# Performance work log

Hardware: AMD Instinct MI355X
Metric: run time of the kernel (lower is better)

Reference implementation:

```python
import jax, jax.numpy as jnp
import numpy as np

B, S, D, E = 32, 16, 64, 768  # batch, max summary segments, max doc splits, embed dim
EPS = 1e-12


def _l2norm(x):
    # tf.nn.l2_normalize: x * rsqrt(max(sum(x^2), eps))
    return x * jax.lax.rsqrt(jnp.maximum(jnp.sum(x * x, axis=-1, keepdims=True), EPS))


def setup_inputs() -> dict:
    key = jax.random.key(0)
    ks = jax.random.split(key, 12)
    nd = jax.random.randint(ks[0], (B,), 1, D + 1)
    ns = jax.random.randint(ks[1], (B,), 1, S + 1)
    doc = jax.random.normal(ks[2], (B, D, E), jnp.float32)
    seg = jax.random.normal(ks[3], (B, S, E), jnp.float32)
    # emulate RaggedTensor.to_tensor(): zero padding beyond ragged lengths
    doc = doc * (jnp.arange(D)[None, :, None] < nd[:, None, None])
    seg = seg * (jnp.arange(S)[None, :, None] < ns[:, None, None])
    tis = jax.random.uniform(ks[4], (B, S), jnp.float32)
    tis = jnp.where(jnp.arange(S)[None, :] < ns[:, None], tis, 1.0)
    tagg = jax.random.uniform(ks[5], (B,), jnp.float32)
    s1, s2, s3 = 1.0 / np.sqrt(2 * E), 1.0 / np.sqrt(E), 1.0 / np.sqrt(E // 2)
    W1 = jax.random.normal(ks[6], (2 * E, E), jnp.float32) * s1
    W2 = jax.random.normal(ks[7], (E, E // 2), jnp.float32) * s2
    W3 = jax.random.normal(ks[8], (E // 2, 1), jnp.float32) * s3
    return {
        'document_splits_embedding': doc,
        'summary_sentences_embedding': seg,
        'num_document_splits': nd,
        'num_summary_segments': ns,
        'target_agg_score': tagg,
        'target_instance_score': tis,
        'W1': W1, 'b1': jnp.zeros((E,), jnp.float32),
        'W2': W2, 'b2': jnp.zeros((E // 2,), jnp.float32),
        'W3': W3, 'b3': jnp.zeros((1,), jnp.float32),
    }


def reference(document_splits_embedding, summary_sentences_embedding,
              num_document_splits, num_summary_segments,
              target_agg_score, target_instance_score,
              W1, b1, W2, b2, W3, b3):
    doc, seg = document_splits_embedding, summary_sentences_embedding
    nd, ns = num_document_splits, num_summary_segments
    b, d, e = doc.shape
    s = seg.shape[1]
    nsf = ns.astype(jnp.float32)

    # target_instance_score padded with 1.0 beyond ragged length (done in setup; pass through)
    tis = target_instance_score

    # ---- pairwise MLP over all (segment, doc_split) pairs ----
    pair = jnp.concatenate([
        jnp.broadcast_to(doc[:, None, :, :], (b, s, d, e)),
        jnp.broadcast_to(seg[:, :, None, :], (b, s, d, e)),
    ], axis=-1)                                             # [B,S,D,2E]
    h = jax.nn.gelu(pair @ W1 + b1, approximate=False)      # [B,S,D,E]
    h = jax.nn.gelu(h @ W2 + b2, approximate=False)         # [B,S,D,E/2]
    mlp_out = jax.nn.sigmoid(h @ W3 + b3)[..., 0]           # [B,S,D]

    doc_mask = (jnp.arange(d)[None, :] < nd[:, None]).astype(jnp.float32)  # [B,D]
    scored = doc_mask[:, None, :] * mlp_out                # mask invalid doc splits
    pred0 = jnp.max(scored, axis=2)                         # [B,S]
    seg_scale = jnp.where(ns > 10, 1.0, 100.0)[:, None]     # faithful to mask+(1-mask)*100
    pred = seg_scale * pred0                                # [B,S]

    # ---- cosine similarity prior (keras CosineSimilarity = -cos) ----
    dn = _l2norm(doc)                                       # [B,D,E]
    sn = _l2norm(seg)                                       # [B,S,E]
    cos = jnp.einsum('bse,bde->bsd', sn, dn)                # [B,S,D]
    sim = doc_mask[:, None, :] * (1.0 + (-cos)) / 2.0
    doc_cos = jnp.max(sim, axis=2)                          # [B,S]
    seg_mask = (jnp.arange(s)[None, :] < ns[:, None]).astype(jnp.float32)
    diff = jnp.abs(doc_cos - pred) * seg_mask
    cos_prior = jnp.mean(jnp.sum(diff, axis=1) / nsf)

    # ---- correlation prior: Pearson correlation over the 768 'sample' axis ----
    c = seg - jnp.mean(seg, axis=-1, keepdims=True)
    z = c * jax.lax.rsqrt(jnp.maximum(jnp.sum(c * c, axis=-1, keepdims=True), EPS))
    R = (1.0 + jnp.einsum('bse,bte->bst', z, z)) / 2.0      # [B,S,S]
    p = pred
    t1 = (1.0 - p)[:, :, None] * (1.0 - p)[:, None, :]
    t2 = p[:, :, None] * p[:, None, :]
    pair_mask = seg_mask[:, :, None] * seg_mask[:, None, :]
    term = jnp.abs(t1 - R) * jnp.abs(t2 - R) * pair_mask
    corr_prior = jnp.mean(jnp.sum(term, axis=(1, 2)) / nsf)

    return (target_agg_score, tis, pred, ns, cos_prior, corr_prior)
```

## Files before the change

### kernel.cpp

```cpp
#include <hip/hip_runtime.h>
#include <hip/hip_bf16.h>
#include <math.h>

#define EPSF 1e-12f

typedef short bf16x8 __attribute__((ext_vector_type(8)));
typedef float f32x4  __attribute__((ext_vector_type(4)));

__device__ __forceinline__ float gelu_fast(float x) {
    float x2 = x * x;
    float z = -2.3021184f * x * fmaf(0.044715f, x2, 1.0f);
    float u = __builtin_amdgcn_exp2f(z);
    return x * __builtin_amdgcn_rcpf(1.0f + u);
}
__device__ __forceinline__ float sigmoid_fast(float x) {
    float u = __builtin_amdgcn_exp2f(-1.44269504f * x);
    return __builtin_amdgcn_rcpf(1.0f + u);
}
__device__ __forceinline__ float bf2f(unsigned short u) {
    return __uint_as_float(((unsigned int)u) << 16);
}
__device__ __forceinline__ unsigned short f2bf(float f) {
    unsigned int u = __float_as_uint(f);
    u += 0x7FFFu + ((u >> 16) & 1u);
// ... 68 lines not shown
        sT[tr][tc4 + i * 4 + 0] = v.x; sT[tr][tc4 + i * 4 + 1] = v.y;
        sT[tr][tc4 + i * 4 + 2] = v.z; sT[tr][tc4 + i * 4 + 3] = v.w;
    }
    __syncthreads();
    union { uint4 v; unsigned short u[8]; } o0, o1;
    #pragma unroll
    for (int i = 0; i < 8; ++i) o0.u[i] = f2bf(sT[tc4 + i][tr]);
    #pragma unroll
    for (int i = 0; i < 8; ++i) o1.u[i] = f2bf(sT[tc4 + 8 + i][tr]);
    *(uint4*)(out2 + (size_t)(c0 + tr) * R + r0 + tc4) = o0.v;
    *(uint4*)(out2 + (size_t)(c0 + tr) * R + r0 + tc4 + 8) = o1.v;
}

__global__ __launch_bounds__(256) void k_l1(
    const unsigned short* __restrict__ docB, const unsigned short* __restrict__ segB,
    const unsigned short* __restrict__ W1T_bf, const float* __restrict__ b1,
    unsigned short* __restrict__ XdocB, unsigned short* __restrict__ XsegB)
{
    int mb = blockIdx.x;
    int n0 = blockIdx.y * 128;
    int t = threadIdx.x, w = t >> 6, l = t & 63;
    int lm = l & 15, kh = l >> 4;
    bool isdoc = (mb < 32);
    int m0 = isdoc ? mb * 64 : (mb - 32) * 64;
    const unsigned short* A = isdoc ? docB : segB;
    int koff = isdoc ? 0 : 768;
    unsigned short* C = isdoc ? XdocB : XsegB;

    const unsigned short* gA = A + (size_t)(m0 + lm) * 768 + kh * 8;
    const unsigned short* gB = W1T_bf + (size_t)(n0 + w * 32 + lm) * 1536 + koff + kh * 8;

    f32x4 acc[4][2];
    #pragma unroll
    for (int mt = 0; mt < 4; ++mt)
        #pragma unroll
        for (int nt = 0; nt < 2; ++nt) acc[mt][nt] = (f32x4){0.f, 0.f, 0.f, 0.f};

    bf16x8 aA[4], aB[4], bA[2], bB[2];
    #pragma unroll
    for (int mt = 0; mt < 4; ++mt) aA[mt] = *(const bf16x8*)(gA + (size_t)mt * 16 * 768);
    #pragma unroll
    for (int nt = 0; nt < 2; ++nt) bA[nt] = *(const bf16x8*)(gB + (size_t)nt * 16 * 1536);

    for (int kt = 0; kt < 12; ++kt) {
        int ko1 = kt * 64 + 32;
        #pragma unroll
        for (int mt = 0; mt < 4; ++mt) aB[mt] = *(const bf16x8*)(gA + (size_t)mt * 16 * 768 + ko1);
        #pragma unroll
        for (int nt = 0; nt < 2; ++nt) bB[nt] = *(const bf16x8*)(gB + (size_t)nt * 16 * 1536 + ko1);
        #pragma unroll
        for (int mt = 0; mt < 4; ++mt)
            #pragma unroll
            for (int nt = 0; nt < 2; ++nt)
                acc[mt][nt] = __builtin_amdgcn_mfma_f32_16x16x32_bf16(
                    aA[mt], bA[nt], acc[mt][nt], 0, 0, 0);
        if (kt < 11) {
            int ko2 = kt * 64 + 64;
            #pragma unroll
            for (int mt = 0; mt < 4; ++mt) aA[mt] = *(const bf16x8*)(gA + (size_t)mt * 16 * 768 + ko2);
            #pragma unroll
            for (int nt = 0; nt < 2; ++nt) bA[nt] = *(const bf16x8*)(gB + (size_t)nt * 16 * 1536 + ko2);
        }
        #pragma unroll
        for (int mt = 0; mt < 4; ++mt)
            #pragma unroll
            for (int nt = 0; nt < 2; ++nt)
                acc[mt][nt] = __builtin_amdgcn_mfma_f32_16x16x32_bf16(
                    aB[mt], bB[nt], acc[mt][nt], 0, 0, 0);
    }
    #pragma unroll
    for (int nt = 0; nt < 2; ++nt) {
        int n = n0 + w * 32 + nt * 16 + lm;
        float bv = isdoc ? 0.f : b1[n];
        #pragma unroll
        for (int mt = 0; mt < 4; ++mt)
            #pragma unroll
            for (int j = 0; j < 4; ++j) {
                int row = m0 + mt * 16 + kh * 4 + j;
                C[(size_t)row * 768 + n] = f2bf(acc[mt][nt][j] + bv);
            }
    }
}

__global__ __launch_bounds__(256, 2) void k_fused_mfma(
    const unsigned short* __restrict__ XdocB, const unsigned short* __restrict__ XsegB,
    const unsigned short* __restrict__ W2T_bf,
    const float* __restrict__ b2, const float* __restrict__ W3, const float* __restrict__ b3,
    const int* __restrict__ nd, const int* __restrict__ ns,
    const unsigned short* __restrict__ docB, const unsigned short* __restrict__ segB,
    const float* __restrict__ seg,
    const float* __restrict__ dscale, const float* __restrict__ sscale,
    const float* __restrict__ smean, const float* __restrict__ cscale,
    float* __restrict__ out_pred, float* __restrict__ predv,
    float* __restrict__ dcws, float* __restrict__ Rws)
{
    __shared__ union {
        struct {
            unsigned short sA0[64 * 64];
            unsigned short sA1[64 * 64];
            float sXseg[768];
            float sRed[64][4];
        } p;
        struct { float sRedC[16][4]; } c;
        struct { unsigned short zb[16][776]; } r;
    } U;

    int blk = blockIdx.x;
    int t = threadIdx.x, w = t >> 6, l = t & 63;
    int lm = l & 15, kh = l >> 4;

    if (blk >= 512) {
        if (blk < 544) {
            int b = blk - 512;
            const unsigned short* gS = segB + (size_t)(b * 16 + lm) * 768 + kh * 8;
            const unsigned short* gD = docB + (size_t)(b * 64 + w * 16 + lm) * 768 + kh * 8;
            f32x4 acc = (f32x4){0.f, 0.f, 0.f, 0.f};
            for (int kt = 0; kt < 24; ++kt) {
                bf16x8 a = *(const bf16x8*)(gS + kt * 32);
                bf16x8 bb = *(const bf16x8*)(gD + kt * 32);
                acc = __builtin_amdgcn_mfma_f32_16x16x32_bf16(a, bb, acc, 0, 0, 0);
            }
            int ndb = nd[b];
            int d = w * 16 + lm;
            float dsc = dscale[b * 64 + d];
            #pragma unroll
            for (int j = 0; j < 4; ++j) {
                int s = kh * 4 + j;
                float cosv = acc[j] * sscale[b * 16 + s] * dsc;
                float sim = (d < ndb) ? (1.0f - cosv) * 0.5f : 0.f;
                sim = fmaxf(sim, __shfl_xor(sim, 1));
                sim = fmaxf(sim, __shfl_xor(sim, 2));
                sim = fmaxf(sim, __shfl_xor(sim, 4));
                sim = fmaxf(sim, __shfl_xor(sim, 8));
                if (lm == 0) U.c.sRedC[s][w] = sim;
            }
            __syncthreads();
            if (t < 16) {
                float dc = fmaxf(fmaxf(U.c.sRedC[t][0], U.c.sRedC[t][1]),
                                 fmaxf(U.c.sRedC[t][2], U.c.sRedC[t][3]));
                dcws[b * 16 + t] = dc;
            }
        } else {
            int b = blk - 544;
            for (int i = t; i < 16 * 768; i += 256) {
                int s = i / 768; int e = i - s * 768;
                U.r.zb[s][e] = f2bf((seg[((size_t)b * 16 + s) * 768 + e]
                                     - smean[b * 16 + s]) * cscale[b * 16 + s]);
            }
            __syncthreads();
            if (w == 0) {
                f32x4 acc = (f32x4){0.f, 0.f, 0.f, 0.f};
                #pragma unroll
                for (int kt = 0; kt < 24; ++kt) {
                    bf16x8 z = *(const bf16x8*)&U.r.zb[lm][kt * 32 + kh * 8];
                    acc = __builtin_amdgcn_mfma_f32_16x16x32_bf16(z, z, acc, 0, 0, 0);
                }
                #pragma unroll
                for (int j = 0; j < 4; ++j) {
                    int row = kh * 4 + j;
                    Rws[b * 256 + row * 16 + lm] = 0.5f * (1.0f + acc[j]);
                }
            }
        }
        return;
    }

    int bs = blk;
    int b = bs >> 4;
    int sw2 = (lm & 7) << 4;

    for (int i = t; i < 768; i += 256) U.p.sXseg[i] = bf2f(XsegB[(size_t)bs * 768 + i]);

    const int ndb = nd[b];
    const float segscale = (ns[b] > 10) ? 1.0f : 100.0f;
    const float b3v = b3[0];

    f32x4 acc[4][6];
    #pragma unroll
    for (int mt = 0; mt < 4; ++mt)
        #pragma unroll
        for (int nt = 0; nt < 6; ++nt) acc[mt][nt] = (f32x4){0.f, 0.f, 0.f, 0.f};

    int ar = t >> 2, ak = (t & 3) * 16;
    int asw = (ar & 7) << 4;
    const char* gXd = (const char*)XdocB + (size_t)(b * 64 + ar) * 1536;
    const unsigned short* gW2w = W2T_bf + (size_t)(w * 96 + lm) * 768 + kh * 8;

    union u128 { uint4 v; unsigned short u[8]; };

    bf16x8 bbA[6], bbB[6];
    #pragma unroll
    for (int nt = 0; nt < 6; ++nt)
        bbA[nt] = *(const bf16x8*)(gW2w + (size_t)nt * 16 * 768);

    {
        u128 xc0, xc1;
        xc0.v = *(const uint4*)(gXd + ak * 2);
        xc1.v = *(const uint4*)(gXd + ak * 2 + 16);
        __syncthreads();
        u128 o0, o1;
        #pragma unroll
        for (int i = 0; i < 8; ++i)
            o0.u[i] = f2bf(gelu_fast(bf2f(xc0.u[i]) + U.p.sXseg[ak + i]));
        #pragma unroll
        for (int i = 0; i < 8; ++i)
            o1.u[i] = f2bf(gelu_fast(bf2f(xc1.u[i]) + U.p.sXseg[ak + 8 + i]));
        *(uint4*)((char*)U.p.sA0 + ar * 128 + ((ak * 2) ^ asw)) = o0.v;
        *(uint4*)((char*)U.p.sA0 + ar * 128 + ((ak * 2 + 16) ^ asw)) = o1.v;
    }

    #pragma unroll
    for (int kt = 0; kt < 12; ++kt) {
        unsigned short* cbuf = (kt & 1) ? U.p.sA1 : U.p.sA0;
        unsigned short* nbuf = (kt & 1) ? U.p.sA0 : U.p.sA1;
        __syncthreads();
        u128 xn0, xn1;
        if (kt < 11) {
            xn0.v = *(const uint4*)(gXd + (kt + 1) * 128 + ak * 2);
            xn1.v = *(const uint4*)(gXd + (kt + 1) * 128 + ak * 2 + 16);
        }
        {
            #pragma unroll
            for (int nt = 0; nt < 6; ++nt)
                bbB[nt] = *(const bf16x8*)(gW2w + (size_t)nt * 16 * 768 + kt * 64 + 32);
            int kb = (kh * 16) ^ sw2;
            bf16x8 a[4];
            #pragma unroll
            for (int mt = 0; mt < 4; ++mt)
                a[mt] = *(const bf16x8*)((const char*)cbuf + (mt * 16 + lm) * 128 + kb);
            #pragma unroll
            for (int mt = 0; mt < 4; ++mt)
                #pragma unroll
                for (int nt = 0; nt < 6; ++nt)
                    acc[mt][nt] = __builtin_amdgcn_mfma_f32_16x16x32_bf16(
                        a[mt], bbA[nt], acc[mt][nt], 0, 0, 0);
        }
        {
            if (kt < 11) {
                #pragma unroll
                for (int nt = 0; nt < 6; ++nt)
                    bbA[nt] = *(const bf16x8*)(gW2w + (size_t)nt * 16 * 768 + (kt + 1) * 64);
            }
            int kb = (64 + kh * 16) ^ sw2;
            bf16x8 a[4];
            #pragma unroll
            for (int mt = 0; mt < 4; ++mt)
                a[mt] = *(const bf16x8*)((const char*)cbuf + (mt * 16 + lm) * 128 + kb);
            #pragma unroll
            for (int mt = 0; mt < 4; ++mt)
                #pragma unroll
                for (int nt = 0; nt < 6; ++nt)
                    acc[mt][nt] = __builtin_amdgcn_mfma_f32_16x16x32_bf16(
                        a[mt], bbB[nt], acc[mt][nt], 0, 0, 0);
        }
        if (kt < 11) {
            u128 o0, o1;
            #pragma unroll
            for (int i = 0; i < 8; ++i)
                o0.u[i] = f2bf(gelu_fast(bf2f(xn0.u[i]) + U.p.sXseg[(kt + 1) * 64 + ak + i]));
            #pragma unroll
            for (int i = 0; i < 8; ++i)
                o1.u[i] = f2bf(gelu_fast(bf2f(xn1.u[i]) + U.p.sXseg[(kt + 1) * 64 + ak + 8 + i]));
            *(uint4*)((char*)nbuf + ar * 128 + ((ak * 2) ^ asw)) = o0.v;
            *(uint4*)((char*)nbuf + ar * 128 + ((ak * 2 + 16) ^ asw)) = o1.v;
        }
    }

    float b2v[6], w3v[6];
    #pragma unroll
    for (int nt = 0; nt < 6; ++nt) {
        int n = w * 96 + nt * 16 + lm;
        b2v[nt] = b2[n]; w3v[nt] = W3[n];
    }
    #pragma unroll
    for (int mt = 0; mt < 4; ++mt) {
        #pragma unroll
        for (int j = 0; j < 4; ++j) {
            float s = 0.f;
            #pragma unroll
            for (int nt = 0; nt < 6; ++nt)
                s += gelu_fast(acc[mt][nt][j] + b2v[nt]) * w3v[nt];
            s += __shfl_xor(s, 1); s += __shfl_xor(s, 2);
            s += __shfl_xor(s, 4); s += __shfl_xor(s, 8);
            if (lm == 0) U.p.sRed[mt * 16 + kh * 4 + j][w] = s;
        }
    }
    __syncthreads();
    if (w == 0) {
        float h3 = U.p.sRed[l][0] + U.p.sRed[l][1] + U.p.sRed[l][2] + U.p.sRed[l][3] + b3v;
        float sig = sigmoid_fast(h3);
        float val = (l < ndb) ? sig : 0.f;
        #pragma unroll
        for (int off = 32; off > 0; off >>= 1) val = fmaxf(val, __shfl_xor(val, off));
        if (l == 0) {
            float pv = segscale * val;
            out_pred[bs] = pv;
            predv[bs] = pv;
        }
    }
}

__global__ __launch_bounds__(256) void k_final(
    const int* __restrict__ ns, const float* __restrict__ dcws,
    const float* __restrict__ Rws, const float* __restrict__ predv,
    float* __restrict__ out)
{
    __shared__ float sl1[32], sl2[32];
    int t = threadIdx.x;
    if (t < 32) {
        int nsb = ns[t];
        float sb = 0.f;
        #pragma unroll
        for (int s = 0; s < 16; ++s) {
            float d = fabsf(dcws[t * 16 + s] - predv[t * 16 + s]);
            sb += (s < nsb) ? d : 0.f;
        }
        sl1[t] = sb / (float)nsb;
    }
    {
        int b = t >> 3, c = t & 7;
        int nsb = ns[b];
        float sum = 0.f;
        #pragma unroll
        for (int k = 0; k < 32; ++k) {
            int idx = c * 32 + k;
            int s = idx >> 4, tt = idx & 15;
            float R = Rws[b * 256 + idx];
            float ps = predv[b * 16 + s], pt = predv[b * 16 + tt];
            float t1 = (1.f - ps) * (1.f - pt), t2 = ps * pt;
            float term = fabsf(t1 - R) * fabsf(t2 - R);
            sum += (s < nsb && tt < nsb) ? term : 0.f;
        }
        sum += __shfl_xor(sum, 1);
        sum += __shfl_xor(sum, 2);
        sum += __shfl_xor(sum, 4);
        if (c == 0) sl2[b] = sum / (float)nsb;
    }
    __syncthreads();
    if (t == 0) {
        float a = 0.f, bsum = 0.f;
        #pragma unroll
        for (int i = 0; i < 32; ++i) { a += sl1[i]; bsum += sl2[i]; }
        out[1088] = a * (1.0f / 32.0f);
        out[1089] = bsum * (1.0f / 32.0f);
    }
}

extern "C" void kernel_launch(void* const* d_in, const int* in_sizes, int n_in,
                              void* d_out, int out_size, void* d_ws, size_t ws_size,
                              hipStream_t stream)
{
    const float* doc  = (const float*)d_in[0];
    const float* seg  = (const float*)d_in[1];
    const int*   nd   = (const int*)d_in[2];
    const int*   ns   = (const int*)d_in[3];
    const float* tagg = (const float*)d_in[4];
    const float* tis  = (const float*)d_in[5];
    const float* W1   = (const float*)d_in[6];
    const float* b1   = (const float*)d_in[7];
    const float* W2   = (const float*)d_in[8];
    const float* b2   = (const float*)d_in[9];
    const float* W3   = (const float*)d_in[10];
    const float* b3   = (const float*)d_in[11];
    float* out = (float*)d_out;

    float* fws      = (float*)d_ws;
    float* dscale   = fws;
    float* sscale   = dscale + 2048;
    float* smean    = sscale + 512;
    float* cscale   = smean + 512;
    float* predv    = cscale + 512;
    float* dcws     = predv + 512;
    float* Rws      = dcws + 512;
    unsigned short* docB  = (unsigned short*)(Rws + 8192);
    unsigned short* segB  = docB + (size_t)2048 * 768;
    unsigned short* W1T   = segB + (size_t)512 * 768;
    unsigned short* W2T   = W1T + (size_t)768 * 1536;
    unsigned short* XdocB = W2T + (size_t)384 * 768;
    unsigned short* XsegB = XdocB + (size_t)2048 * 768;

    k_prep<<<1001, 256, 0, stream>>>(doc, seg, W1, W2, tagg, tis, ns,
                                     dscale, sscale, smean, cscale,
                                     docB, segB, W1T, W2T, out);
    k_l1<<<dim3(40, 6), 256, 0, stream>>>(docB, segB, W1T, b1, XdocB, XsegB);
    k_fused_mfma<<<576, 256, 0, stream>>>(XdocB, XsegB, W2T, b2, W3, b3, nd, ns,
                                          docB, segB, seg, dscale, sscale,
                                          smean, cscale, out + 544, predv,
                                          dcws, Rws);
    k_final<<<1, 256, 0, stream>>>(ns, dcws, Rws, predv, out);
}
```

Baseline: 83.98 us.

## Stage full GELU hidden tile in LDS and split N across 8 waves

The fused second-layer kernel now uses 512 threads. It computes the whole 64x768 GELU(Xdoc+Xseg) activation tile into LDS in one pass before the MFMA loop, replacing the per-k-step double-buffered staging that needed a barrier every iteration. Each of the 8 waves now covers 48 output columns instead of 96, which halves the accumulator registers per wave, and the W2 fragments stay register double-buffered. The cost is a 96KB LDS tile per block, which limits how many blocks fit on a CU, plus a serial prologue before any MFMA work starts. The auxiliary cosine and correlation blocks move to the front of the grid.

```diff
diff --git a/kernel.cpp b/kernel.cpp
--- a/kernel.cpp
+++ b/kernel.cpp
@@ -174,7 +174,7 @@
     }
 }
 
-__global__ __launch_bounds__(256, 2) void k_fused_mfma(
+__global__ __launch_bounds__(512, 2) void k_fused_mfma(
     const unsigned short* __restrict__ XdocB, const unsigned short* __restrict__ XsegB,
     const unsigned short* __restrict__ W2T_bf,
     const float* __restrict__ b2, const float* __restrict__ W3, const float* __restrict__ b3,
@@ -186,24 +186,17 @@
     float* __restrict__ out_pred, float* __restrict__ predv,
     float* __restrict__ dcws, float* __restrict__ Rws)
 {
-    __shared__ union {
-        struct {
-            unsigned short sA0[64 * 64];
-            unsigned short sA1[64 * 64];
-            float sXseg[768];
-            float sRed[64][4];
-        } p;
-        struct { float sRedC[16][4]; } c;
-        struct { unsigned short zb[16][776]; } r;
-    } U;
+    __shared__ unsigned short sH1[64 * 768];
+    __shared__ float sRed[64][8];
 
     int blk = blockIdx.x;
     int t = threadIdx.x, w = t >> 6, l = t & 63;
     int lm = l & 15, kh = l >> 4;
-
-    if (blk >= 512) {
-        if (blk < 544) {
-            int b = blk - 512;
+    union u128 { uint4 v; unsigned short u[8]; };
+
+    if (blk < 32) {
+        int b = blk;
+        if (w < 4) {
             const unsigned short* gS = segB + (size_t)(b * 16 + lm) * 768 + kh * 8;
             const unsigned short* gD = docB + (size_t)(b * 64 + w * 16 + lm) * 768 + kh * 8;
             f32x4 acc = (f32x4){0.f, 0.f, 0.f, 0.f};
@@ -224,144 +217,120 @@
                 sim = fmaxf(sim, __shfl_xor(sim, 2));
                 sim = fmaxf(sim, __shfl_xor(sim, 4));
                 sim = fmaxf(sim, __shfl_xor(sim, 8));
-                if (lm == 0) U.c.sRedC[s][w] = sim;
-            }
-            __syncthreads();
-            if (t < 16) {
-                float dc = fmaxf(fmaxf(U.c.sRedC[t][0], U.c.sRedC[t][1]),
-                                 fmaxf(U.c.sRedC[t][2], U.c.sRedC[t][3]));
-                dcws[b * 16 + t] = dc;
-            }
-        } else {
-            int b = blk - 544;
-            for (int i = t; i < 16 * 768; i += 256) {
-                int s = i / 768; int e = i - s * 768;
-                U.r.zb[s][e] = f2bf((seg[((size_t)b * 16 + s) * 768 + e]
-                                     - smean[b * 16 + s]) * cscale[b * 16 + s]);
-            }
-            __syncthreads();
-            if (w == 0) {
-                f32x4 acc = (f32x4){0.f, 0.f, 0.f, 0.f};
-                #pragma unroll
-                for (int kt = 0; kt < 24; ++kt) {
-                    bf16x8 z = *(const bf16x8*)&U.r.zb[lm][kt * 32 + kh * 8];
-                    acc = __builtin_amdgcn_mfma_f32_16x16x32_bf16(z, z, acc, 0, 0, 0);
-                }
-                #pragma unroll
-                for (int j = 0; j < 4; ++j) {
-                    int row = kh * 4 + j;
-                    Rws[b * 256 + row * 16 + lm] = 0.5f * (1.0f + acc[j]);
-                }
-            }
+                if (lm == 0) sRed[s][w] = sim;
+            }
+        }
+        __syncthreads();
+        if (t < 16) {
+            float dc = fmaxf(fmaxf(sRed[t][0], sRed[t][1]),
+                             fmaxf(sRed[t][2], sRed[t][3]));
+            dcws[b * 16 + t] = dc;
         }
         return;
     }
-
-    int bs = blk;
+    if (blk < 64) {
+        int b = blk - 32;
+        unsigned short* zb = sH1;
+        for (int i = t; i < 16 * 768; i += 512) {
+            int s = i / 768; int e = i - s * 768;
+            zb[s * 776 + e] = f2bf((seg[((size_t)b * 16 + s) * 768 + e]
+                                    - smean[b * 16 + s]) * cscale[b * 16 + s]);
+        }
+        __syncthreads();
+        if (w == 0) {
+            f32x4 acc = (f32x4){0.f, 0.f, 0.f, 0.f};
+            #pragma unroll
+            for (int kt = 0; kt < 24; ++kt) {
+                bf16x8 z = *(const bf16x8*)&zb[lm * 776 + kt * 32 + kh * 8];
+                acc = __builtin_amdgcn_mfma_f32_16x16x32_bf16(z, z, acc, 0, 0, 0);
+            }
+            #pragma unroll
+            for (int j = 0; j < 4; ++j) {
+                int row = kh * 4 + j;
+                Rws[b * 256 + row * 16 + lm] = 0.5f * (1.0f + acc[j]);
+            }
+        }
+        return;
+    }
+
+    int bs = blk - 64;
     int b = bs >> 4;
-    int sw2 = (lm & 7) << 4;
-
-    for (int i = t; i < 768; i += 256) U.p.sXseg[i] = bf2f(XsegB[(size_t)bs * 768 + i]);
-
     const int ndb = nd[b];
     const float segscale = (ns[b] > 10) ? 1.0f : 100.0f;
     const float b3v = b3[0];
 
-    f32x4 acc[4][6];
+    {
+        int r = t >> 3, ci = t & 7;
+        int rsw = (r & 7) << 4;
+        const unsigned short* gXd = XdocB + (size_t)(b * 64 + r) * 768;
+        const unsigned short* gXs = XsegB + (size_t)bs * 768;
+        #pragma unroll
+        for (int i = 0; i < 12; ++i) {
+            int c = i * 8 + ci;
+            int k0 = c * 8;
+            u128 xd, xs, o;
+            xd.v = *(const uint4*)(gXd + k0);
+            xs.v = *(const uint4*)(gXs + k0);
+            #pragma unroll
+            for (int j = 0; j < 8; ++j)
+                o.u[j] = f2bf(gelu_fast(bf2f(xd.u[j]) + bf2f(xs.u[j])));
+            *(uint4*)((char*)sH1 + r * 1536 + ((c * 16) ^ rsw)) = o.v;
+        }
+    }
+    __syncthreads();
+
+    f32x4 acc[4][3];
     #pragma unroll
     for (int mt = 0; mt < 4; ++mt)
         #pragma unroll
-        for (int nt = 0; nt < 6; ++nt) acc[mt][nt] = (f32x4){0.f, 0.f, 0.f, 0.f};
-
-    int ar = t >> 2, ak = (t & 3) * 16;
-    int asw = (ar & 7) << 4;
-    const char* gXd = (const char*)XdocB + (size_t)(b * 64 + ar) * 1536;
-    const unsigned short* gW2w = W2T_bf + (size_t)(w * 96 + lm) * 768 + kh * 8;
-
-    union u128 { uint4 v; unsigned short u[8]; };
-
-    bf16x8 bbA[6], bbB[6];
-    #pragma unroll
-    for (int nt = 0; nt < 6; ++nt)
-        bbA[nt] = *(const bf16x8*)(gW2w + (size_t)nt * 16 * 768);
-
-    {
-        u128 xc0, xc1;
-        xc0.v = *(const uint4*)(gXd + ak * 2);
-        xc1.v = *(const uint4*)(gXd + ak * 2 + 16);
-        __syncthreads();
-        u128 o0, o1;
-        #pragma unroll
-        for (int i = 0; i < 8; ++i)
-            o0.u[i] = f2bf(gelu_fast(bf2f(xc0.u[i]) + U.p.sXseg[ak + i]));
-        #pragma unroll
-        for (int i = 0; i < 8; ++i)
-            o1.u[i] = f2bf(gelu_fast(bf2f(xc1.u[i]) + U.p.sXseg[ak + 8 + i]));
-        *(uint4*)((char*)U.p.sA0 + ar * 128 + ((ak * 2) ^ asw)) = o0.v;
-        *(uint4*)((char*)U.p.sA0 + ar * 128 + ((ak * 2 + 16) ^ asw)) = o1.v;
-    }
-
-    #pragma unroll
-    for (int kt = 0; kt < 12; ++kt) {
-        unsigned short* cbuf = (kt & 1) ? U.p.sA1 : U.p.sA0;
-        unsigned short* nbuf = (kt & 1) ? U.p.sA0 : U.p.sA1;
-        __syncthreads();
-        u128 xn0, xn1;
-        if (kt < 11) {
-            xn0.v = *(const uint4*)(gXd + (kt + 1) * 128 + ak * 2);
-            xn1.v = *(const uint4*)(gXd + (kt + 1) * 128 + ak * 2 + 16);
-        }
-        {
-            #pragma unroll
-            for (int nt = 0; nt < 6; ++nt)
-                bbB[nt] = *(const bf16x8*)(gW2w + (size_t)nt * 16 * 768 + kt * 64 + 32);
-            int kb = (kh * 16) ^ sw2;
-            bf16x8 a[4];
-            #pragma unroll
-            for (int mt = 0; mt < 4; ++mt)
-                a[mt] = *(const bf16x8*)((const char*)cbuf + (mt * 16 + lm) * 128 + kb);
-            #pragma unroll
-            for (int mt = 0; mt < 4; ++mt)
-                #pragma unroll
-                for (int nt = 0; nt < 6; ++nt)
-                    acc[mt][nt] = __builtin_amdgcn_mfma_f32_16x16x32_bf16(
-                        a[mt], bbA[nt], acc[mt][nt], 0, 0, 0);
-        }
-        {
-            if (kt < 11) {
-                #pragma unroll
-                for (int nt = 0; nt < 6; ++nt)
-                    bbA[nt] = *(const bf16x8*)(gW2w + (size_t)nt * 16 * 768 + (kt + 1) * 64);
-            }
-            int kb = (64 + kh * 16) ^ sw2;
-            bf16x8 a[4];
-            #pragma unroll
-            for (int mt = 0; mt < 4; ++mt)
-                a[mt] = *(const bf16x8*)((const char*)cbuf + (mt * 16 + lm) * 128 + kb);
-            #pragma unroll
-            for (int mt = 0; mt < 4; ++mt)
-                #pragma unroll
-                for (int nt = 0; nt < 6; ++nt)
-                    acc[mt][nt] = __builtin_amdgcn_mfma_f32_16x16x32_bf16(
-                        a[mt], bbB[nt], acc[mt][nt], 0, 0, 0);
-        }
-        if (kt < 11) {
-            u128 o0, o1;
-            #pragma unroll
-            for (int i = 0; i < 8; ++i)
-                o0.u[i] = f2bf(gelu_fast(bf2f(xn0.u[i]) + U.p.sXseg[(kt + 1) * 64 + ak + i]));
-            #pragma unroll
-            for (int i = 0; i < 8; ++i)
-                o1.u[i] = f2bf(gelu_fast(bf2f(xn1.u[i]) + U.p.sXseg[(kt + 1) * 64 + ak + 8 + i]));
-            *(uint4*)((char*)nbuf + ar * 128 + ((ak * 2) ^ asw)) = o0.v;
-            *(uint4*)((char*)nbuf + ar * 128 + ((ak * 2 + 16) ^ asw)) = o1.v;
-        }
-    }
-
-    float b2v[6], w3v[6];
-    #pragma unroll
-    for (int nt = 0; nt < 6; ++nt) {
-        int n = w * 96 + nt * 16 + lm;
+        for (int nt = 0; nt < 3; ++nt) acc[mt][nt] = (f32x4){0.f, 0.f, 0.f, 0.f};
+
+    const unsigned short* gW2w = W2T_bf + (size_t)(w * 48 + lm) * 768 + kh * 8;
+    int asw = (lm & 7) << 4;
+
+    bf16x8 bA_[6], bB_[6];
+    #pragma unroll
+    for (int j = 0; j < 6; ++j)
+        bA_[j] = *(const bf16x8*)(gW2w + (size_t)(j % 3) * 16 * 768 + (j / 3) * 32);
+
+    #define KT_BODY(KT, CUR, NXT)                                               \
+    {                                                                           \
+        if ((KT) < 11) {                                                        \
+            _Pragma("unroll")                                                   \
+            for (int j_ = 0; j_ < 6; ++j_)                                      \
+                NXT[j_] = *(const bf16x8*)(gW2w + (size_t)(j_ % 3) * 16 * 768   \
+                                           + ((KT) + 1) * 64 + (j_ / 3) * 32);  \
+        }                                                                       \
+        _Pragma("unroll")                                                       \
+        for (int kk = 0; kk < 2; ++kk) {                                        \
+            int koff = (KT) * 128 + kk * 64 + kh * 16;                          \
+            bf16x8 a_[4];                                                       \
+            _Pragma("unroll")                                                   \
+            for (int mt = 0; mt < 4; ++mt)                                      \
+                a_[mt] = *(const bf16x8*)((const char*)sH1                      \
+                            + (mt * 16 + lm) * 1536 + (koff ^ asw));            \
+            _Pragma("unroll")                                                   \
+            for (int mt = 0; mt < 4; ++mt) {                                    \
+                acc[mt][0] = __builtin_amdgcn_mfma_f32_16x16x32_bf16(           \
+                    a_[mt], CUR[kk * 3 + 0], acc[mt][0], 0, 0, 0);              \
+                acc[mt][1] = __builtin_amdgcn_mfma_f32_16x16x32_bf16(           \
+                    a_[mt], CUR[kk * 3 + 1], acc[mt][1], 0, 0, 0);              \
+                acc[mt][2] = __builtin_amdgcn_mfma_f32_16x16x32_bf16(           \
+                    a_[mt], CUR[kk * 3 + 2], acc[mt][2], 0, 0, 0);              \
+            }                                                                   \
+        }                                                                       \
+    }
+
+    for (int kt2 = 0; kt2 < 12; kt2 += 2) {
+        KT_BODY(kt2,     bA_, bB_);
+        KT_BODY(kt2 + 1, bB_, bA_);
+    }
+    #undef KT_BODY
+
+    float b2v[3], w3v[3];
+    #pragma unroll
+    for (int nt = 0; nt < 3; ++nt) {
+        int n = w * 48 + nt * 16 + lm;
         b2v[nt] = b2[n]; w3v[nt] = W3[n];
     }
     #pragma unroll
@@ -370,16 +339,18 @@
         for (int j = 0; j < 4; ++j) {
             float s = 0.f;
             #pragma unroll
-            for (int nt = 0; nt < 6; ++nt)
+            for (int nt = 0; nt < 3; ++nt)
                 s += gelu_fast(acc[mt][nt][j] + b2v[nt]) * w3v[nt];
             s += __shfl_xor(s, 1); s += __shfl_xor(s, 2);
             s += __shfl_xor(s, 4); s += __shfl_xor(s, 8);
-            if (lm == 0) U.p.sRed[mt * 16 + kh * 4 + j][w] = s;
+            if (lm == 0) sRed[mt * 16 + kh * 4 + j][w] = s;
         }
     }
     __syncthreads();
     if (w == 0) {
-        float h3 = U.p.sRed[l][0] + U.p.sRed[l][1] + U.p.sRed[l][2] + U.p.sRed[l][3] + b3v;
+        float h3 = b3v;
+        #pragma unroll
+        for (int j = 0; j < 8; ++j) h3 += sRed[l][j];
         float sig = sigmoid_fast(h3);
         float val = (l < ndb) ? sig : 0.f;
         #pragma unroll
@@ -475,7 +446,7 @@
                                      dscale, sscale, smean, cscale,
                                      docB, segB, W1T, W2T, out);
     k_l1<<<dim3(40, 6), 256, 0, stream>>>(docB, segB, W1T, b1, XdocB, XsegB);
-    k_fused_mfma<<<576, 256, 0, stream>>>(XdocB, XsegB, W2T, b2, W3, b3, nd, ns,
+    k_fused_mfma<<<576, 512, 0, stream>>>(XdocB, XsegB, W2T, b2, W3, b3, nd, ns,
                                           docB, segB, seg, dscale, sscale,
                                           smean, cscale, out + 544, predv,
                                           dcws, Rws);
```

New measurement: 93.96 us. +11.9%, slower.

## Split fused MLP blocks into doc halves and precompute GELU tile in LDS

Applied to the files above, without the earlier changes.

Each (batch, segment) block of the second-layer MLP is split into two blocks that each cover 32 document rows, doubling the grid to 1088 blocks. Each block computes the full GELU activation tile into LDS up front instead of double-buffering per k-step, which removes per-iteration barriers. Launch bounds rise to 3 blocks per CU. The cos and correlation blocks move to the front of the grid, and a block-index remap interleaves the half-tiles. The max over the two halves and the per-batch scale move into the final kernel. In exchange, the W2 weights are re-read twice as often and each block uses a larger LDS footprint.

```diff
diff --git a/kernel.cpp b/kernel.cpp
--- a/kernel.cpp
+++ b/kernel.cpp
@@ -174,24 +174,21 @@
     }
 }
 
-__global__ __launch_bounds__(256, 2) void k_fused_mfma(
+__global__ __launch_bounds__(256, 3) void k_fused_mfma(
     const unsigned short* __restrict__ XdocB, const unsigned short* __restrict__ XsegB,
     const unsigned short* __restrict__ W2T_bf,
     const float* __restrict__ b2, const float* __restrict__ W3, const float* __restrict__ b3,
-    const int* __restrict__ nd, const int* __restrict__ ns,
+    const int* __restrict__ nd,
     const unsigned short* __restrict__ docB, const unsigned short* __restrict__ segB,
     const float* __restrict__ seg,
     const float* __restrict__ dscale, const float* __restrict__ sscale,
     const float* __restrict__ smean, const float* __restrict__ cscale,
-    float* __restrict__ out_pred, float* __restrict__ predv,
-    float* __restrict__ dcws, float* __restrict__ Rws)
+    float* __restrict__ predhalf, float* __restrict__ dcws, float* __restrict__ Rws)
 {
     __shared__ union {
         struct {
-            unsigned short sA0[64 * 64];
-            unsigned short sA1[64 * 64];
-            float sXseg[768];
-            float sRed[64][4];
+            unsigned short sH1[32 * 768];
+            float sRed[32][4];
         } p;
         struct { float sRedC[16][4]; } c;
         struct { unsigned short zb[16][776]; } r;
@@ -200,132 +197,123 @@
     int blk = blockIdx.x;
     int t = threadIdx.x, w = t >> 6, l = t & 63;
     int lm = l & 15, kh = l >> 4;
-
-    if (blk >= 512) {
-        if (blk < 544) {
-            int b = blk - 512;
-            const unsigned short* gS = segB + (size_t)(b * 16 + lm) * 768 + kh * 8;
-            const unsigned short* gD = docB + (size_t)(b * 64 + w * 16 + lm) * 768 + kh * 8;
+    union u128 { uint4 v; unsigned short u[8]; };
+
+    if (blk < 32) {
+        int b = blk;
+        const unsigned short* gS = segB + (size_t)(b * 16 + lm) * 768 + kh * 8;
+        const unsigned short* gD = docB + (size_t)(b * 64 + w * 16 + lm) * 768 + kh * 8;
+        f32x4 acc = (f32x4){0.f, 0.f, 0.f, 0.f};
+        for (int kt = 0; kt < 24; ++kt) {
+            bf16x8 a = *(const bf16x8*)(gS + kt * 32);
+            bf16x8 bb = *(const bf16x8*)(gD + kt * 32);
+            acc = __builtin_amdgcn_mfma_f32_16x16x32_bf16(a, bb, acc, 0, 0, 0);
+        }
+        int ndb = nd[b];
+        int d = w * 16 + lm;
+        float dsc = dscale[b * 64 + d];
+        #pragma unroll
+        for (int j = 0; j < 4; ++j) {
+            int s = kh * 4 + j;
+            float cosv = acc[j] * sscale[b * 16 + s] * dsc;
+            float sim = (d < ndb) ? (1.0f - cosv) * 0.5f : 0.f;
+            sim = fmaxf(sim, __shfl_xor(sim, 1));
+            sim = fmaxf(sim, __shfl_xor(sim, 2));
+            sim = fmaxf(sim, __shfl_xor(sim, 4));
+            sim = fmaxf(sim, __shfl_xor(sim, 8));
+            if (lm == 0) U.c.sRedC[s][w] = sim;
+        }
+        __syncthreads();
+        if (t < 16) {
+            float dc = fmaxf(fmaxf(U.c.sRedC[t][0], U.c.sRedC[t][1]),
+                             fmaxf(U.c.sRedC[t][2], U.c.sRedC[t][3]));
+            dcws[b * 16 + t] = dc;
+        }
+        return;
+    }
+    if (blk < 64) {
+        int b = blk - 32;
+        for (int i = t; i < 16 * 768; i += 256) {
+            int s = i / 768; int e = i - s * 768;
+            U.r.zb[s][e] = f2bf((seg[((size_t)b * 16 + s) * 768 + e]
+                                 - smean[b * 16 + s]) * cscale[b * 16 + s]);
+        }
+        __syncthreads();
+        if (w == 0) {
             f32x4 acc = (f32x4){0.f, 0.f, 0.f, 0.f};
+            #pragma unroll
             for (int kt = 0; kt < 24; ++kt) {
-                bf16x8 a = *(const bf16x8*)(gS + kt * 32);
-                bf16x8 bb = *(const bf16x8*)(gD + kt * 32);
-                acc = __builtin_amdgcn_mfma_f32_16x16x32_bf16(a, bb, acc, 0, 0, 0);
+                bf16x8 z = *(const bf16x8*)&U.r.zb[lm][kt * 32 + kh * 8];
+                acc = __builtin_amdgcn_mfma_f32_16x16x32_bf16(z, z, acc, 0, 0, 0);
             }
-            int ndb = nd[b];
-            int d = w * 16 + lm;
-            float dsc = dscale[b * 64 + d];
             #pragma unroll
             for (int j = 0; j < 4; ++j) {
-                int s = kh * 4 + j;
-                float cosv = acc[j] * sscale[b * 16 + s] * dsc;
-                float sim = (d < ndb) ? (1.0f - cosv) * 0.5f : 0.f;
-                sim = fmaxf(sim, __shfl_xor(sim, 1));
-                sim = fmaxf(sim, __shfl_xor(sim, 2));
-                sim = fmaxf(sim, __shfl_xor(sim, 4));
-                sim = fmaxf(sim, __shfl_xor(sim, 8));
-                if (lm == 0) U.c.sRedC[s][w] = sim;
+                int row = kh * 4 + j;
+                Rws[b * 256 + row * 16 + lm] = 0.5f * (1.0f + acc[j]);
             }
-            __syncthreads();
-            if (t < 16) {
-                float dc = fmaxf(fmaxf(U.c.sRedC[t][0], U.c.sRedC[t][1]),
-                                 fmaxf(U.c.sRedC[t][2], U.c.sRedC[t][3]));
-                dcws[b * 16 + t] = dc;
-            }
-        } else {
-            int b = blk - 544;
-            for (int i = t; i < 16 * 768; i += 256) {
-                int s = i / 768; int e = i - s * 768;
-                U.r.zb[s][e] = f2bf((seg[((size_t)b * 16 + s) * 768 + e]
-                                     - smean[b * 16 + s]) * cscale[b * 16 + s]);
-            }
-            __syncthreads();
-            if (w == 0) {
-                f32x4 acc = (f32x4){0.f, 0.f, 0.f, 0.f};
-                #pragma unroll
-                for (int kt = 0; kt < 24; ++kt) {
-                    bf16x8 z = *(const bf16x8*)&U.r.zb[lm][kt * 32 + kh * 8];
-                    acc = __builtin_amdgcn_mfma_f32_16x16x32_bf16(z, z, acc, 0, 0, 0);
-                }
-                #pragma unroll
-                for (int j = 0; j < 4; ++j) {
-                    int row = kh * 4 + j;
-                    Rws[b * 256 + row * 16 + lm] = 0.5f * (1.0f + acc[j]);
-                }
-            }
         }
         return;
     }
 
-    int bs = blk;
+    int p = blk - 64;
+    int lidx = (p & 7) * 128 + (p >> 3);
+    int half = lidx & 1;
+    int bs = lidx >> 1;
     int b = bs >> 4;
-    int sw2 = (lm & 7) << 4;
-
-    for (int i = t; i < 768; i += 256) U.p.sXseg[i] = bf2f(XsegB[(size_t)bs * 768 + i]);
-
     const int ndb = nd[b];
-    const float segscale = (ns[b] > 10) ? 1.0f : 100.0f;
-    const float b3v = b3[0];
-
-    f32x4 acc[4][6];
-    #pragma unroll
-    for (int mt = 0; mt < 4; ++mt)
+
+    {
+        int r = t >> 3, ci = t & 7;
+        int rsw = (r & 7) << 4;
+        const unsigned short* gXd = XdocB + (size_t)(b * 64 + half * 32 + r) * 768;
+        const unsigned short* gXs = XsegB + (size_t)bs * 768;
+        #pragma unroll
+        for (int i = 0; i < 12; ++i) {
+            int c = i * 8 + ci;
+            int k0 = c * 8;
+            u128 xd, xs, o;
+            xd.v = *(const uint4*)(gXd + k0);
+            xs.v = *(const uint4*)(gXs + k0);
+            #pragma unroll
+            for (int j = 0; j < 8; ++j)
+                o.u[j] = f2bf(gelu_fast(bf2f(xd.u[j]) + bf2f(xs.u[j])));
+            *(uint4*)((char*)U.p.sH1 + r * 1536 + ((c * 16) ^ rsw)) = o.v;
+        }
+    }
+    __syncthreads();
+
+    f32x4 acc[2][6];
+    #pragma unroll
+    for (int mt = 0; mt < 2; ++mt)
         #pragma unroll
         for (int nt = 0; nt < 6; ++nt) acc[mt][nt] = (f32x4){0.f, 0.f, 0.f, 0.f};
 
-    int ar = t >> 2, ak = (t & 3) * 16;
-    int asw = (ar & 7) << 4;
-    const char* gXd = (const char*)XdocB + (size_t)(b * 64 + ar) * 1536;
     const unsigned short* gW2w = W2T_bf + (size_t)(w * 96 + lm) * 768 + kh * 8;
-
-    union u128 { uint4 v; unsigned short u[8]; };
+    int asw = (lm & 7) << 4;
 
     bf16x8 bbA[6], bbB[6];
     #pragma unroll
     for (int nt = 0; nt < 6; ++nt)
         bbA[nt] = *(const bf16x8*)(gW2w + (size_t)nt * 16 * 768);
 
-    {
-        u128 xc0, xc1;
-        xc0.v = *(const uint4*)(gXd + ak * 2);
-        xc1.v = *(const uint4*)(gXd + ak * 2 + 16);
-        __syncthreads();
-        u128 o0, o1;
-        #pragma unroll
-        for (int i = 0; i < 8; ++i)
-            o0.u[i] = f2bf(gelu_fast(bf2f(xc0.u[i]) + U.p.sXseg[ak + i]));
-        #pragma unroll
-        for (int i = 0; i < 8; ++i)
-            o1.u[i] = f2bf(gelu_fast(bf2f(xc1.u[i]) + U.p.sXseg[ak + 8 + i]));
-        *(uint4*)((char*)U.p.sA0 + ar * 128 + ((ak * 2) ^ asw)) = o0.v;
-        *(uint4*)((char*)U.p.sA0 + ar * 128 + ((ak * 2 + 16) ^ asw)) = o1.v;
-    }
-
     #pragma unroll
     for (int kt = 0; kt < 12; ++kt) {
-        unsigned short* cbuf = (kt & 1) ? U.p.sA1 : U.p.sA0;
-        unsigned short* nbuf = (kt & 1) ? U.p.sA0 : U.p.sA1;
-        __syncthreads();
-        u128 xn0, xn1;
-        if (kt < 11) {
-            xn0.v = *(const uint4*)(gXd + (kt + 1) * 128 + ak * 2);
-            xn1.v = *(const uint4*)(gXd + (kt + 1) * 128 + ak * 2 + 16);
-        }
         {
             #pragma unroll
             for (int nt = 0; nt < 6; ++nt)
                 bbB[nt] = *(const bf16x8*)(gW2w + (size_t)nt * 16 * 768 + kt * 64 + 32);
-            int kb = (kh * 16) ^ sw2;
-            bf16x8 a[4];
-            #pragma unroll
-            for (int mt = 0; mt < 4; ++mt)
-                a[mt] = *(const bf16x8*)((const char*)cbuf + (mt * 16 + lm) * 128 + kb);
-            #pragma unroll
-            for (int mt = 0; mt < 4; ++mt)
+            int koff = kt * 128 + kh * 16;
+            bf16x8 a_[2];
+            #pragma unroll
+            for (int mt = 0; mt < 2; ++mt)
+                a_[mt] = *(const bf16x8*)((const char*)U.p.sH1
+                            + (mt * 16 + lm) * 1536 + (koff ^ asw));
+            #pragma unroll
+            for (int mt = 0; mt < 2; ++mt)
                 #pragma unroll
                 for (int nt = 0; nt < 6; ++nt)
                     acc[mt][nt] = __builtin_amdgcn_mfma_f32_16x16x32_bf16(
-                        a[mt], bbA[nt], acc[mt][nt], 0, 0, 0);
+                        a_[mt], bbA[nt], acc[mt][nt], 0, 0, 0);
         }
         {
             if (kt < 11) {
@@ -333,28 +321,18 @@
                 for (int nt = 0; nt < 6; ++nt)
                     bbA[nt] = *(const bf16x8*)(gW2w + (size_t)nt * 16 * 768 + (kt + 1) * 64);
             }
-            int kb = (64 + kh * 16) ^ sw2;
-            bf16x8 a[4];
-            #pragma unroll
-            for (int mt = 0; mt < 4; ++mt)
-                a[mt] = *(const bf16x8*)((const char*)cbuf + (mt * 16 + lm) * 128 + kb);
-            #pragma unroll
-            for (int mt = 0; mt < 4; ++mt)
+            int koff = kt * 128 + 64 + kh * 16;
+            bf16x8 a_[2];
+            #pragma unroll
+            for (int mt = 0; mt < 2; ++mt)
+                a_[mt] = *(const bf16x8*)((const char*)U.p.sH1
+                            + (mt * 16 + lm) * 1536 + (koff ^ asw));
+            #pragma unroll
+            for (int mt = 0; mt < 2; ++mt)
                 #pragma unroll
                 for (int nt = 0; nt < 6; ++nt)
                     acc[mt][nt] = __builtin_amdgcn_mfma_f32_16x16x32_bf16(
-                        a[mt], bbB[nt], acc[mt][nt], 0, 0, 0);
-        }
-        if (kt < 11) {
-            u128 o0, o1;
-            #pragma unroll
-            for (int i = 0; i < 8; ++i)
-                o0.u[i] = f2bf(gelu_fast(bf2f(xn0.u[i]) + U.p.sXseg[(kt + 1) * 64 + ak + i]));
-            #pragma unroll
-            for (int i = 0; i < 8; ++i)
-                o1.u[i] = f2bf(gelu_fast(bf2f(xn1.u[i]) + U.p.sXseg[(kt + 1) * 64 + ak + 8 + i]));
-            *(uint4*)((char*)nbuf + ar * 128 + ((ak * 2) ^ asw)) = o0.v;
-            *(uint4*)((char*)nbuf + ar * 128 + ((ak * 2 + 16) ^ asw)) = o1.v;
+                        a_[mt], bbB[nt], acc[mt][nt], 0, 0, 0);
         }
     }
 
@@ -365,7 +343,7 @@
         b2v[nt] = b2[n]; w3v[nt] = W3[n];
     }
     #pragma unroll
-    for (int mt = 0; mt < 4; ++mt) {
+    for (int mt = 0; mt < 2; ++mt) {
         #pragma unroll
         for (int j = 0; j < 4; ++j) {
             float s = 0.f;
@@ -379,32 +357,42 @@
     }
     __syncthreads();
     if (w == 0) {
-        float h3 = U.p.sRed[l][0] + U.p.sRed[l][1] + U.p.sRed[l][2] + U.p.sRed[l][3] + b3v;
-        float sig = sigmoid_fast(h3);
-        float val = (l < ndb) ? sig : 0.f;
-        #pragma unroll
-        for (int off = 32; off > 0; off >>= 1) val = fmaxf(val, __shfl_xor(val, off));
-        if (l == 0) {
-            float pv = segscale * val;
-            out_pred[bs] = pv;
-            predv[bs] = pv;
-        }
+        float val = 0.f;
+        if (l < 32) {
+            float h3 = U.p.sRed[l][0] + U.p.sRed[l][1] + U.p.sRed[l][2]
+                     + U.p.sRed[l][3] + b3[0];
+            float sig = sigmoid_fast(h3);
+            int d = half * 32 + l;
+            val = (d < ndb) ? sig : 0.f;
+        }
+        #pragma unroll
+        for (int off = 16; off > 0; off >>= 1) val = fmaxf(val, __shfl_xor(val, off));
+        if (l == 0) predhalf[half * 512 + bs] = val;
     }
 }
 
 __global__ __launch_bounds__(256) void k_final(
     const int* __restrict__ ns, const float* __restrict__ dcws,
-    const float* __restrict__ Rws, const float* __restrict__ predv,
+    const float* __restrict__ Rws, const float* __restrict__ predhalf,
     float* __restrict__ out)
 {
+    __shared__ float sP[512];
     __shared__ float sl1[32], sl2[32];
     int t = threadIdx.x;
+    for (int i = t; i < 512; i += 256) {
+        int b = i >> 4;
+        float scale = (ns[b] > 10) ? 1.0f : 100.0f;
+        float pv = scale * fmaxf(predhalf[i], predhalf[512 + i]);
+        sP[i] = pv;
+        out[544 + i] = pv;
+    }
+    __syncthreads();
     if (t < 32) {
         int nsb = ns[t];
         float sb = 0.f;
         #pragma unroll
         for (int s = 0; s < 16; ++s) {
-            float d = fabsf(dcws[t * 16 + s] - predv[t * 16 + s]);
+            float d = fabsf(dcws[t * 16 + s] - sP[t * 16 + s]);
             sb += (s < nsb) ? d : 0.f;
         }
         sl1[t] = sb / (float)nsb;
@@ -418,7 +406,7 @@
             int idx = c * 32 + k;
             int s = idx >> 4, tt = idx & 15;
             float R = Rws[b * 256 + idx];
-            float ps = predv[b * 16 + s], pt = predv[b * 16 + tt];
+            float ps = sP[b * 16 + s], pt = sP[b * 16 + tt];
             float t1 = (1.f - ps) * (1.f - pt), t2 = ps * pt;
             float term = fabsf(t1 - R) * fabsf(t2 - R);
             sum += (s < nsb && tt < nsb) ? term : 0.f;
@@ -461,8 +449,8 @@
     float* sscale   = dscale + 2048;
     float* smean    = sscale + 512;
     float* cscale   = smean + 512;
-    float* predv    = cscale + 512;
-    float* dcws     = predv + 512;
+    float* predhalf = cscale + 512;
+    float* dcws     = predhalf + 1024;
     float* Rws      = dcws + 512;
     unsigned short* docB  = (unsigned short*)(Rws + 8192);
     unsigned short* segB  = docB + (size_t)2048 * 768;
@@ -475,9 +463,8 @@
                                      dscale, sscale, smean, cscale,
                                      docB, segB, W1T, W2T, out);
     k_l1<<<dim3(40, 6), 256, 0, stream>>>(docB, segB, W1T, b1, XdocB, XsegB);
-    k_fused_mfma<<<576, 256, 0, stream>>>(XdocB, XsegB, W2T, b2, W3, b3, nd, ns,
-                                          docB, segB, seg, dscale, sscale,
-                                          smean, cscale, out + 544, predv,
-                                          dcws, Rws);
-    k_final<<<1, 256, 0, stream>>>(ns, dcws, Rws, predv, out);
-}
+    k_fused_mfma<<<1088, 256, 0, stream>>>(XdocB, XsegB, W2T, b2, W3, b3, nd,
+                                           docB, segB, seg, dscale, sscale,
+                                           smean, cscale, predhalf, dcws, Rws);
+    k_final<<<1, 256, 0, stream>>>(ns, dcws, Rws, predhalf, out);
+}
```

After: 114.6 us. +36.4%, slower.

## Double fused MLP block to 512 threads and schedule side blocks first

Applied to the files above, without the earlier changes.

The fused layer-2/3 MLP kernel now runs with 512 threads (8 waves) per block. Each wave covers 48 output columns instead of 96, so per-thread accumulators drop from 24 to 12 MFMA tiles, and each thread stages one 16-byte chunk of the GELU'd A tile instead of two. The cosine-prior and correlation-prior blocks are moved to the front of the grid (block ids 0-63) so they start first rather than trailing after the 512 main blocks. The aim is more waves per CU and lower register pressure to hide latency, at the cost of more block-wide syncs over more threads and idle waves in the side blocks.

```diff
diff --git a/kernel.cpp b/kernel.cpp
--- a/kernel.cpp
+++ b/kernel.cpp
@@ -174,7 +174,7 @@
     }
 }
 
-__global__ __launch_bounds__(256, 2) void k_fused_mfma(
+__global__ __launch_bounds__(512, 4) void k_fused_mfma(
     const unsigned short* __restrict__ XdocB, const unsigned short* __restrict__ XsegB,
     const unsigned short* __restrict__ W2T_bf,
     const float* __restrict__ b2, const float* __restrict__ W3, const float* __restrict__ b3,
@@ -191,7 +191,7 @@
             unsigned short sA0[64 * 64];
             unsigned short sA1[64 * 64];
             float sXseg[768];
-            float sRed[64][4];
+            float sRed[64][8];
         } p;
         struct { float sRedC[16][4]; } c;
         struct { unsigned short zb[16][776]; } r;
@@ -200,10 +200,11 @@
     int blk = blockIdx.x;
     int t = threadIdx.x, w = t >> 6, l = t & 63;
     int lm = l & 15, kh = l >> 4;
-
-    if (blk >= 512) {
-        if (blk < 544) {
-            int b = blk - 512;
+    union u128 { uint4 v; unsigned short u[8]; };
+
+    if (blk < 32) {
+        int b = blk;
+        if (w < 4) {
             const unsigned short* gS = segB + (size_t)(b * 16 + lm) * 768 + kh * 8;
             const unsigned short* gD = docB + (size_t)(b * 64 + w * 16 + lm) * 768 + kh * 8;
             f32x4 acc = (f32x4){0.f, 0.f, 0.f, 0.f};
@@ -226,79 +227,74 @@
                 sim = fmaxf(sim, __shfl_xor(sim, 8));
                 if (lm == 0) U.c.sRedC[s][w] = sim;
             }
-            __syncthreads();
-            if (t < 16) {
-                float dc = fmaxf(fmaxf(U.c.sRedC[t][0], U.c.sRedC[t][1]),
-                                 fmaxf(U.c.sRedC[t][2], U.c.sRedC[t][3]));
-                dcws[b * 16 + t] = dc;
-            }
-        } else {
-            int b = blk - 544;
-            for (int i = t; i < 16 * 768; i += 256) {
-                int s = i / 768; int e = i - s * 768;
-                U.r.zb[s][e] = f2bf((seg[((size_t)b * 16 + s) * 768 + e]
-                                     - smean[b * 16 + s]) * cscale[b * 16 + s]);
-            }
-            __syncthreads();
-            if (w == 0) {
-                f32x4 acc = (f32x4){0.f, 0.f, 0.f, 0.f};
-                #pragma unroll
-                for (int kt = 0; kt < 24; ++kt) {
-                    bf16x8 z = *(const bf16x8*)&U.r.zb[lm][kt * 32 + kh * 8];
-                    acc = __builtin_amdgcn_mfma_f32_16x16x32_bf16(z, z, acc, 0, 0, 0);
-                }
-                #pragma unroll
-                for (int j = 0; j < 4; ++j) {
-                    int row = kh * 4 + j;
-                    Rws[b * 256 + row * 16 + lm] = 0.5f * (1.0f + acc[j]);
-                }
-            }
+        }
+        __syncthreads();
+        if (t < 16) {
+            float dc = fmaxf(fmaxf(U.c.sRedC[t][0], U.c.sRedC[t][1]),
+                             fmaxf(U.c.sRedC[t][2], U.c.sRedC[t][3]));
+            dcws[blk * 16 + t] = dc;
         }
         return;
     }
-
-    int bs = blk;
+    if (blk < 64) {
+        int b = blk - 32;
+        for (int i = t; i < 16 * 768; i += 512) {
+            int s = i / 768; int e = i - s * 768;
+            U.r.zb[s][e] = f2bf((seg[((size_t)b * 16 + s) * 768 + e]
+                                 - smean[b * 16 + s]) * cscale[b * 16 + s]);
+        }
+        __syncthreads();
+        if (w == 0) {
+            f32x4 acc = (f32x4){0.f, 0.f, 0.f, 0.f};
+            #pragma unroll
+            for (int kt = 0; kt < 24; ++kt) {
+                bf16x8 z = *(const bf16x8*)&U.r.zb[lm][kt * 32 + kh * 8];
+                acc = __builtin_amdgcn_mfma_f32_16x16x32_bf16(z, z, acc, 0, 0, 0);
+            }
+            #pragma unroll
+            for (int j = 0; j < 4; ++j) {
+                int row = kh * 4 + j;
+                Rws[b * 256 + row * 16 + lm] = 0.5f * (1.0f + acc[j]);
+            }
+        }
+        return;
+    }
+
+    int bs = blk - 64;
     int b = bs >> 4;
     int sw2 = (lm & 7) << 4;
 
-    for (int i = t; i < 768; i += 256) U.p.sXseg[i] = bf2f(XsegB[(size_t)bs * 768 + i]);
+    for (int i = t; i < 768; i += 512) U.p.sXseg[i] = bf2f(XsegB[(size_t)bs * 768 + i]);
 
     const int ndb = nd[b];
     const float segscale = (ns[b] > 10) ? 1.0f : 100.0f;
     const float b3v = b3[0];
 
-    f32x4 acc[4][6];
+    f32x4 acc[4][3];
     #pragma unroll
     for (int mt = 0; mt < 4; ++mt)
         #pragma unroll
-        for (int nt = 0; nt < 6; ++nt) acc[mt][nt] = (f32x4){0.f, 0.f, 0.f, 0.f};
-
-    int ar = t >> 2, ak = (t & 3) * 16;
+        for (int nt = 0; nt < 3; ++nt) acc[mt][nt] = (f32x4){0.f, 0.f, 0.f, 0.f};
+
+    int ar = t >> 3, ci = t & 7;
     int asw = (ar & 7) << 4;
     const char* gXd = (const char*)XdocB + (size_t)(b * 64 + ar) * 1536;
-    const unsigned short* gW2w = W2T_bf + (size_t)(w * 96 + lm) * 768 + kh * 8;
-
-    union u128 { uint4 v; unsigned short u[8]; };
-
-    bf16x8 bbA[6], bbB[6];
-    #pragma unroll
-    for (int nt = 0; nt < 6; ++nt)
+    const unsigned short* gW2w = W2T_bf + (size_t)(w * 48 + lm) * 768 + kh * 8;
+
+    bf16x8 bbA[3], bbB[3];
+    #pragma unroll
+    for (int nt = 0; nt < 3; ++nt)
         bbA[nt] = *(const bf16x8*)(gW2w + (size_t)nt * 16 * 768);
 
     {
-        u128 xc0, xc1;
-        xc0.v = *(const uint4*)(gXd + ak * 2);
-        xc1.v = *(const uint4*)(gXd + ak * 2 + 16);
+        u128 xc;
+        xc.v = *(const uint4*)(gXd + ci * 16);
         __syncthreads();
-        u128 o0, o1;
+        u128 o;
         #pragma unroll
         for (int i = 0; i < 8; ++i)
-            o0.u[i] = f2bf(gelu_fast(bf2f(xc0.u[i]) + U.p.sXseg[ak + i]));
-        #pragma unroll
-        for (int i = 0; i < 8; ++i)
-            o1.u[i] = f2bf(gelu_fast(bf2f(xc1.u[i]) + U.p.sXseg[ak + 8 + i]));
-        *(uint4*)((char*)U.p.sA0 + ar * 128 + ((ak * 2) ^ asw)) = o0.v;
-        *(uint4*)((char*)U.p.sA0 + ar * 128 + ((ak * 2 + 16) ^ asw)) = o1.v;
+            o.u[i] = f2bf(gelu_fast(bf2f(xc.u[i]) + U.p.sXseg[ci * 8 + i]));
+        *(uint4*)((char*)U.p.sA0 + ar * 128 + ((ci * 16) ^ asw)) = o.v;
     }
 
     #pragma unroll
@@ -306,14 +302,11 @@
         unsigned short* cbuf = (kt & 1) ? U.p.sA1 : U.p.sA0;
         unsigned short* nbuf = (kt & 1) ? U.p.sA0 : U.p.sA1;
         __syncthreads();
-        u128 xn0, xn1;
-        if (kt < 11) {
-            xn0.v = *(const uint4*)(gXd + (kt + 1) * 128 + ak * 2);
-            xn1.v = *(const uint4*)(gXd + (kt + 1) * 128 + ak * 2 + 16);
-        }
+        u128 xn;
+        if (kt < 11) xn.v = *(const uint4*)(gXd + (kt + 1) * 128 + ci * 16);
         {
             #pragma unroll
-            for (int nt = 0; nt < 6; ++nt)
+            for (int nt = 0; nt < 3; ++nt)
                 bbB[nt] = *(const bf16x8*)(gW2w + (size_t)nt * 16 * 768 + kt * 64 + 32);
             int kb = (kh * 16) ^ sw2;
             bf16x8 a[4];
@@ -323,14 +316,14 @@
             #pragma unroll
             for (int mt = 0; mt < 4; ++mt)
                 #pragma unroll
-                for (int nt = 0; nt < 6; ++nt)
+                for (int nt = 0; nt < 3; ++nt)
                     acc[mt][nt] = __builtin_amdgcn_mfma_f32_16x16x32_bf16(
                         a[mt], bbA[nt], acc[mt][nt], 0, 0, 0);
         }
         {
             if (kt < 11) {
                 #pragma unroll
-                for (int nt = 0; nt < 6; ++nt)
+                for (int nt = 0; nt < 3; ++nt)
                     bbA[nt] = *(const bf16x8*)(gW2w + (size_t)nt * 16 * 768 + (kt + 1) * 64);
             }
             int kb = (64 + kh * 16) ^ sw2;
@@ -341,27 +334,23 @@
             #pragma unroll
             for (int mt = 0; mt < 4; ++mt)
                 #pragma unroll
-                for (int nt = 0; nt < 6; ++nt)
+                for (int nt = 0; nt < 3; ++nt)
                     acc[mt][nt] = __builtin_amdgcn_mfma_f32_16x16x32_bf16(
                         a[mt], bbB[nt], acc[mt][nt], 0, 0, 0);
         }
         if (kt < 11) {
-            u128 o0, o1;
+            u128 o;
             #pragma unroll
             for (int i = 0; i < 8; ++i)
-                o0.u[i] = f2bf(gelu_fast(bf2f(xn0.u[i]) + U.p.sXseg[(kt + 1) * 64 + ak + i]));
-            #pragma unroll
-            for (int i = 0; i < 8; ++i)
-                o1.u[i] = f2bf(gelu_fast(bf2f(xn1.u[i]) + U.p.sXseg[(kt + 1) * 64 + ak + 8 + i]));
-            *(uint4*)((char*)nbuf + ar * 128 + ((ak * 2) ^ asw)) = o0.v;
-            *(uint4*)((char*)nbuf + ar * 128 + ((ak * 2 + 16) ^ asw)) = o1.v;
-        }
-    }
-
-    float b2v[6], w3v[6];
-    #pragma unroll
-    for (int nt = 0; nt < 6; ++nt) {
-        int n = w * 96 + nt * 16 + lm;
+                o.u[i] = f2bf(gelu_fast(bf2f(xn.u[i]) + U.p.sXseg[(kt + 1) * 64 + ci * 8 + i]));
+            *(uint4*)((char*)nbuf + ar * 128 + ((ci * 16) ^ asw)) = o.v;
+        }
+    }
+
+    float b2v[3], w3v[3];
+    #pragma unroll
+    for (int nt = 0; nt < 3; ++nt) {
+        int n = w * 48 + nt * 16 + lm;
         b2v[nt] = b2[n]; w3v[nt] = W3[n];
     }
     #pragma unroll
@@ -370,7 +359,7 @@
         for (int j = 0; j < 4; ++j) {
             float s = 0.f;
             #pragma unroll
-            for (int nt = 0; nt < 6; ++nt)
+            for (int nt = 0; nt < 3; ++nt)
                 s += gelu_fast(acc[mt][nt][j] + b2v[nt]) * w3v[nt];
             s += __shfl_xor(s, 1); s += __shfl_xor(s, 2);
             s += __shfl_xor(s, 4); s += __shfl_xor(s, 8);
@@ -379,7 +368,9 @@
     }
     __syncthreads();
     if (w == 0) {
-        float h3 = U.p.sRed[l][0] + U.p.sRed[l][1] + U.p.sRed[l][2] + U.p.sRed[l][3] + b3v;
+        float h3 = U.p.sRed[l][0] + U.p.sRed[l][1] + U.p.sRed[l][2] + U.p.sRed[l][3]
+                 + U.p.sRed[l][4] + U.p.sRed[l][5] + U.p.sRed[l][6] + U.p.sRed[l][7]
+                 + b3v;
         float sig = sigmoid_fast(h3);
         float val = (l < ndb) ? sig : 0.f;
         #pragma unroll
@@ -475,7 +466,7 @@
                                      dscale, sscale, smean, cscale,
                                      docB, segB, W1T, W2T, out);
     k_l1<<<dim3(40, 6), 256, 0, stream>>>(docB, segB, W1T, b1, XdocB, XsegB);
-    k_fused_mfma<<<576, 256, 0, stream>>>(XdocB, XsegB, W2T, b2, W3, b3, nd, ns,
+    k_fused_mfma<<<576, 512, 0, stream>>>(XdocB, XsegB, W2T, b2, W3, b3, nd, ns,
                                           docB, segB, seg, dscale, sscale,
                                           smean, cscale, out + 544, predv,
                                           dcws, Rws);
```

Result: slower. 87.69 us (+4.4%).
